# Optimization experiments

Measured on AMD Instinct MI355X. Metric: run time of the kernel, lower is better.

The kernel has to match this reference:

```python
import jax, jax.numpy as jnp
import numpy as np

NUM_HEADS = 16

def _alibi(S, H, dtype):
    # fairseq-style ALiBi: slopes[h] * -(|i-j|), H assumed power of 2
    start = 2.0 ** (-8.0 / H)
    slopes = start ** jnp.arange(1, H + 1, dtype=jnp.float32)      # [H]
    pos = jnp.arange(S)
    rel = -jnp.abs(pos[None, :] - pos[:, None]).astype(jnp.float32)  # [S,S]
    return (slopes[:, None, None] * rel).astype(dtype)             # [H,S,S]

def setup_inputs() -> dict:
    key = jax.random.key(0)
    kx, km, kw1, kw2 = jax.random.split(key, 4)
    B, S, D = 2, 2048, 1024
    inputs = jax.random.normal(kx, (B, S, D), dtype=jnp.float32)
    mask = jax.random.bernoulli(km, 0.9, (B, S))
    mask = mask.at[:, 0].set(True)  # ensure each row has a valid key
    Wqkv = jax.random.normal(kw1, (3 * D, D), dtype=jnp.float32) * 0.02
    bqkv = jnp.zeros((3 * D,), dtype=jnp.float32)
    Wproj = jax.random.normal(kw2, (D, D), dtype=jnp.float32) * 0.02
    bproj = jnp.zeros((D,), dtype=jnp.float32)
    return {"inputs": inputs, "mask": mask, "Wqkv": Wqkv, "bqkv": bqkv,
            "Wproj": Wproj, "bproj": bproj}

def reference(inputs, mask, Wqkv, bqkv, Wproj, bproj):
    B, S, D = inputs.shape
    H = NUM_HEADS
    dh = D // H
    scale = D ** (-0.5)  # NOTE: original scales by full dim, not head dim
    qkv = inputs @ Wqkv.T + bqkv                       # [B,S,3D]
    qkv = qkv.reshape(B, S, H, 3 * dh).transpose(0, 2, 1, 3)  # [B,H,S,3dh]
    q, k, v = qkv[..., :dh], qkv[..., dh:2 * dh], qkv[..., 2 * dh:]
    attn = jnp.einsum('bhqd,bhkd->bhqk', q, k) * scale  # [B,H,S,S]
    attn = attn + _alibi(S, H, attn.dtype)[None]
    attn = jnp.where(mask[:, None, None, :], attn, jnp.finfo(attn.dtype).min)
    attn = jax.nn.softmax(attn, axis=-1)
    x = jnp.einsum('bhqk,bhkd->bhqd', attn, v)          # [B,H,S,dh]
    x = x.transpose(0, 2, 1, 3).reshape(B, S, D)
    return x @ Wproj.T + bproj
```

## Files before the change

kernel.cpp:

```cpp
#include <hip/hip_runtime.h>
#include <cstdint>
#include <cstddef>

#define B_  2
#define S_  2048
#define D_  1024
#define H_  16
#define DH_ 64
#define M_  (B_*S_)
#define N3_ (3*D_)
#define NT_ (S_/64)

typedef float f32x4 __attribute__((ext_vector_type(4)));
typedef short short8 __attribute__((ext_vector_type(8)));
typedef unsigned short u16x8 __attribute__((ext_vector_type(8)));
typedef unsigned short u16x4 __attribute__((ext_vector_type(4)));

__device__ __forceinline__ unsigned short f2bf(float x) {
    unsigned int u = __float_as_uint(x);
    unsigned int r = (u + 0x7FFFu + ((u >> 16) & 1u)) >> 16;
    return (unsigned short)r;
}

__device__ __forceinline__ float exp2_(float x) { return __builtin_amdgcn_exp2f(x); }

__device__ __forceinline__ unsigned int cvt_pk_bf16(float a, float b) {
    unsigned int r;
    asm volatile("v_cvt_pk_bf16_f32 %0, %1, %2" : "=v"(r) : "v"(a), "v"(b));
    return r;
}

__device__ __forceinline__ void gload16(const void* g, void* l) {
    __builtin_amdgcn_global_load_lds(
        (const __attribute__((address_space(1))) unsigned int*)g,
        (__attribute__((address_space(3))) unsigned int*)l,
        16, 0, 0);
}

__global__ void k_detect_mask(const unsigned char* __restrict__ mb, int* __restrict__ flag) {
    __shared__ int sBig, sM4, sM8;
    if (threadIdx.x == 0) { sBig = 0; sM4 = 0; sM8 = 0; }
    __syncthreads();
    int big = 0, m4 = 0, m8 = 0;
    for (int i = threadIdx.x; i < 4096; i += blockDim.x) {
        unsigned char v = mb[i];
        if (v > 1) big = 1;
        if (v && (i & 3)) m4 = 1;
        if (v && ((i & 7) == 4)) m8 = 1;
    }
    if (big) atomicOr(&sBig, 1);
    if (m4)  atomicOr(&sM4, 1);
    if (m8)  atomicOr(&sM8, 1);
    __syncthreads();
    if (threadIdx.x == 0) {
        int w;
        if (sBig)      w = 0;
        else if (sM4)  w = 1;
        else if (sM8)  w = 4;
        else           w = 8;
        *flag = w;
    }
}

__global__ void k_maskbits(const void* __restrict__ mask, const int* __restrict__ flag,
                           unsigned long long* __restrict__ bits) {
    int i = blockIdx.x * 64 + threadIdx.x;
    int w = *flag;
    bool on;
    if (w == 0)      on = ((const float*)mask)[i] != 0.0f;
    else if (w == 1) on = ((const unsigned char*)mask)[i] != 0;
    else if (w == 4) on = ((const int*)mask)[i] != 0;
    else             on = ((const long long*)mask)[i] != 0;
    unsigned long long bal = __ballot(on);
    if (threadIdx.x == 0) bits[blockIdx.x] = bal;
}

__global__ void k_f2bf(const float* __restrict__ in, unsigned short* __restrict__ out, int n) {
    int i = (blockIdx.x * blockDim.x + threadIdx.x) * 4;
    if (i >= n) return;
    float4 v = *reinterpret_cast<const float4*>(&in[i]);
    u16x4 o = { f2bf(v.x), f2bf(v.y), f2bf(v.z), f2bf(v.w) };
    *reinterpret_cast<u16x4*>(&out[i]) = o;
}

template <bool OUT_BF16>
__global__ __launch_bounds__(256) void k_gemm_bf16_nt(
    const unsigned short* __restrict__ A, const unsigned short* __restrict__ W,
    const float* __restrict__ bias, void* __restrict__ Cout,
    int M, int N, int K) {
    __shared__ __align__(16) unsigned short Al[128 * 64];
    __shared__ __align__(16) unsigned short Wl[128 * 64];

    const int tid  = threadIdx.x;
    const int lane = tid & 63;
    const int w    = tid >> 6;
    const int wr   = w >> 1, wc = w & 1;
    const int l16  = lane & 15, g = lane >> 4;
    const int m0 = blockIdx.y * 128, n0 = blockIdx.x * 128;

    f32x4 acc[4][4];
#pragma unroll
    for (int m = 0; m < 4; ++m)
#pragma unroll
        for (int n = 0; n < 4; ++n) acc[m][n] = (f32x4){0.f, 0.f, 0.f, 0.f};

    const int srow = tid >> 3, scol = (tid & 7) * 8;

    for (int k0 = 0; k0 < K; k0 += 64) {
        __syncthreads();
#pragma unroll
        for (int i = 0; i < 4; ++i) {
            const int c = i * 256 + tid;
            const int row = srow + i * 32;
            gload16(A + (size_t)(m0 + row) * K + k0 + scol, Al + c * 8);
            gload16(W + (size_t)(n0 + row) * K + k0 + scol, Wl + c * 8);
        }
        __syncthreads();

#pragma unroll
        for (int kk = 0; kk < 2; ++kk) {
            short8 a[4], b[4];
#pragma unroll
            for (int m = 0; m < 4; ++m)
                a[m] = *reinterpret_cast<const short8*>(
                    &Al[(size_t)(wr * 64 + m * 16 + l16) * 64 + kk * 32 + g * 8]);
#pragma unroll
            for (int n = 0; n < 4; ++n)
                b[n] = *reinterpret_cast<const short8*>(
                    &Wl[(size_t)(wc * 64 + n * 16 + l16) * 64 + kk * 32 + g * 8]);
#pragma unroll
            for (int m = 0; m < 4; ++m)
#pragma unroll
                for (int n = 0; n < 4; ++n)
                    acc[m][n] = __builtin_amdgcn_mfma_f32_16x16x32_bf16(a[m], b[n], acc[m][n], 0, 0, 0);
        }
    }

    float bv[4];
#pragma unroll
    for (int n = 0; n < 4; ++n) bv[n] = bias[n0 + wc * 64 + n * 16 + l16];
#pragma unroll
    for (int m = 0; m < 4; ++m) {
#pragma unroll
        for (int r = 0; r < 4; ++r) {
            const size_t row = m0 + wr * 64 + m * 16 + g * 4 + r;
#pragma unroll
            for (int n = 0; n < 4; ++n) {
                const int col = n0 + wc * 64 + n * 16 + l16;
                float v = acc[m][n][r] + bv[n];
                if (OUT_BF16)
                    ((unsigned short*)Cout)[row * N + col] = f2bf(v);
                else
                    ((float*)Cout)[row * N + col] = v;
            }
        }
    }
}

__global__ __launch_bounds__(256) void k_attn_mfma(
    const unsigned short* __restrict__ qkv,
    const unsigned long long* __restrict__ mbits,
    unsigned short* __restrict__ x) {
    __shared__ __align__(16) unsigned short Kt[64][72];
    __shared__ __align__(16) unsigned short Vt[64][72];
    __shared__ __align__(16) unsigned short QP[64][72];
    __shared__ __align__(16) float Am[S_];

    const int tid  = threadIdx.x;
    const int lane = tid & 63;
    const int wq   = tid >> 6;
    const int g    = lane >> 4;
    const int g4   = g * 4;
    const int l16  = lane & 15;

    const int nqt = S_ / 64;
    const int qt = blockIdx.x % nqt;
    const int h  = (blockIdx.x / nqt) % H_;
    const int b  = blockIdx.x / (nqt * H_);
    const int q0 = qt * 64;
    const size_t rowbase = (size_t)b * S_ * N3_;
    const int hq = h * 192, hk = hq + 64, hv = hq + 128;
    const unsigned short* kvb = qkv + rowbase;

    {
#pragma unroll
        for (int it = 0; it < S_ / 256; ++it) {
            const int k = it * 256 + tid;
            const unsigned long long w = mbits[b * NT_ + (k >> 6)];
            Am[k] = ((w >> (k & 63)) & 1ull) ? 0.0f : -1e30f;
        }
    }

    {
        const int row = tid >> 2, cb = (tid & 3) * 16;
        const unsigned short* src = kvb + (size_t)(q0 + row) * N3_ + hq + cb;
        *reinterpret_cast<u16x8*>(&QP[row][cb])     = *reinterpret_cast<const u16x8*>(src);
        *reinterpret_cast<u16x8*>(&QP[row][cb + 8]) = *reinterpret_cast<const u16x8*>(src + 8);
    }
    __syncthreads();

    const short8 qa0 = *reinterpret_cast<const short8*>(&QP[wq*16 + l16][g*8]);
    const short8 qa1 = *reinterpret_cast<const short8*>(&QP[wq*16 + l16][32 + g*8]);

    f32x4 Oacc[4];
#pragma unroll
    for (int df = 0; df < 4; ++df) Oacc[df] = (f32x4){0.f, 0.f, 0.f, 0.f};
    float m = -1e30f, l = 0.0f;

    const float LOG2E = 1.4426950408889634f;
    const float c1 = 0.03125f * LOG2E;
    const float c2 = exp2f(-0.5f * (float)(h + 1)) * LOG2E;
    const int   qg = q0 + wq * 16 + l16;
    float albr[4];
#pragma unroll
    for (int r = 0; r < 4; ++r) albr[r] = c2 * (float)(g4 + r);
    const float c2_16 = c2 * 16.0f;

    const int krow = tid >> 2, kcb = (tid & 3) * 16;
    const int vkb = (tid & 15) * 4, vdb = (tid >> 4) * 4;
    u16x8 kr0, kr1;
    u16x4 vr0, vr1, vr2, vr3;

    {
        const unsigned short* ks = kvb + (size_t)krow * N3_ + hk + kcb;
        kr0 = *reinterpret_cast<const u16x8*>(ks);
        kr1 = *reinterpret_cast<const u16x8*>(ks + 8);
        const unsigned short* vs = kvb + (size_t)vkb * N3_ + hv + vdb;
        vr0 = *reinterpret_cast<const u16x4*>(vs);
        vr1 = *reinterpret_cast<const u16x4*>(vs + N3_);
        vr2 = *reinterpret_cast<const u16x4*>(vs + 2 * N3_);
        vr3 = *reinterpret_cast<const u16x4*>(vs + 3 * N3_);
    }

    for (int t = 0; t < NT_; ++t) {
        const int k0 = t * 64;
        __syncthreads();

        *reinterpret_cast<u16x8*>(&Kt[krow][kcb])     = kr0;
        *reinterpret_cast<u16x8*>(&Kt[krow][kcb + 8]) = kr1;
        {
            u16x4 w0 = { vr0.x, vr1.x, vr2.x, vr3.x };
            u16x4 w1 = { vr0.y, vr1.y, vr2.y, vr3.y };
            u16x4 w2 = { vr0.z, vr1.z, vr2.z, vr3.z };
            u16x4 w3 = { vr0.w, vr1.w, vr2.w, vr3.w };
            *reinterpret_cast<u16x4*>(&Vt[vdb + 0][vkb]) = w0;
            *reinterpret_cast<u16x4*>(&Vt[vdb + 1][vkb]) = w1;
            *reinterpret_cast<u16x4*>(&Vt[vdb + 2][vkb]) = w2;
            *reinterpret_cast<u16x4*>(&Vt[vdb + 3][vkb]) = w3;
        }
        if (t + 1 < NT_) {
            const int kn = k0 + 64;
            const unsigned short* ks = kvb + (size_t)(kn + krow) * N3_ + hk + kcb;
            kr0 = *reinterpret_cast<const u16x8*>(ks);
            kr1 = *reinterpret_cast<const u16x8*>(ks + 8);
            const unsigned short* vs = kvb + (size_t)(kn + vkb) * N3_ + hv + vdb;
            vr0 = *reinterpret_cast<const u16x4*>(vs);
            vr1 = *reinterpret_cast<const u16x4*>(vs + N3_);
            vr2 = *reinterpret_cast<const u16x4*>(vs + 2 * N3_);
            vr3 = *reinterpret_cast<const u16x4*>(vs + 3 * N3_);
        }
        __syncthreads();

        float p_[4][4];
        __builtin_amdgcn_s_setprio(1);
#pragma unroll
        for (int jb = 0; jb < 4; ++jb) {
            short8 kb0 = *reinterpret_cast<const short8*>(&Kt[jb*16 + l16][g*8]);
            short8 kb1 = *reinterpret_cast<const short8*>(&Kt[jb*16 + l16][32 + g*8]);
            f32x4 c = (f32x4){0.f, 0.f, 0.f, 0.f};
            c = __builtin_amdgcn_mfma_f32_16x16x32_bf16(kb0, qa0, c, 0, 0, 0);
            c = __builtin_amdgcn_mfma_f32_16x16x32_bf16(kb1, qa1, c, 0, 0, 0);
#pragma unroll
            for (int r = 0; r < 4; ++r) p_[jb][r] = c[r];
        }
        __builtin_amdgcn_s_setprio(0);

        f32x4 amv[4];
#pragma unroll
        for (int jb = 0; jb < 4; ++jb)
            amv[jb] = *reinterpret_cast<const f32x4*>(&Am[k0 + jb * 16 + g4]);

        if (k0 < q0) {
            const float tb = c2 * (float)(k0 - qg);
#pragma unroll
            for (int jb = 0; jb < 4; ++jb) {
                const float tbj = tb + c2_16 * (float)jb;
#pragma unroll
                for (int r = 0; r < 4; ++r)
                    p_[jb][r] = fmaf(p_[jb][r], c1, tbj + albr[r] + amv[jb][r]);
            }
        } else if (k0 > q0) {
            const float tb = c2 * (float)(k0 - qg);
#pragma unroll
            for (int jb = 0; jb < 4; ++jb) {
                const float tbj = -tb - c2_16 * (float)jb;
#pragma unroll
                for (int r = 0; r < 4; ++r)
                    p_[jb][r] = fmaf(p_[jb][r], c1, tbj - albr[r] + amv[jb][r]);
            }
        } else {
            const int dbase = k0 - qg;
#pragma unroll
            for (int jb = 0; jb < 4; ++jb)
#pragma unroll
                for (int r = 0; r < 4; ++r) {
                    int d = dbase + jb * 16 + g4 + r;
                    d = d < 0 ? -d : d;
                    p_[jb][r] = fmaf(p_[jb][r], c1, amv[jb][r] - c2 * (float)d);
                }
        }

        float mx;
        {
            float m0_ = fmaxf(fmaxf(p_[0][0], p_[0][1]), fmaxf(p_[0][2], p_[0][3]));
            float m1_ = fmaxf(fmaxf(p_[1][0], p_[1][1]), fmaxf(p_[1][2], p_[1][3]));
            float m2_ = fmaxf(fmaxf(p_[2][0], p_[2][1]), fmaxf(p_[2][2], p_[2][3]));
            float m3_ = fmaxf(fmaxf(p_[3][0], p_[3][1]), fmaxf(p_[3][2], p_[3][3]));
            mx = fmaxf(fmaxf(m0_, m1_), fmaxf(m2_, m3_));
        }
        mx = fmaxf(mx, __shfl_xor(mx, 16));
        mx = fmaxf(mx, __shfl_xor(mx, 32));

        if (__any(mx > m + 8.0f)) {
            const float mn = fmaxf(m, mx);
            const float cr = exp2_(m - mn);
            m = mn;
            l *= cr;
            const int srcb = (lane & 48) + ((lane & 48) >> 2);
#pragma unroll
            for (int r = 0; r < 4; ++r) {
                const float crq = __shfl(cr, srcb + r);
#pragma unroll
                for (int df = 0; df < 4; ++df) Oacc[df][r] *= crq;
            }
        }

        float ps = 0.0f;
#pragma unroll
        for (int jb = 0; jb < 4; ++jb)
#pragma unroll
            for (int r = 0; r < 4; ++r) {
                float p = exp2_(p_[jb][r] - m);
                p_[jb][r] = p;
                ps += p;
            }

#pragma unroll
        for (int jb = 0; jb < 4; ++jb) {
            uint2 st;
            st.x = cvt_pk_bf16(p_[jb][0], p_[jb][1]);
            st.y = cvt_pk_bf16(p_[jb][2], p_[jb][3]);
            *reinterpret_cast<uint2*>(&QP[wq*16 + l16][jb*16 + g4]) = st;
        }

        const short8 pa0 = *reinterpret_cast<const short8*>(&QP[wq*16 + l16][g*8]);
        const short8 pa1 = *reinterpret_cast<const short8*>(&QP[wq*16 + l16][32 + g*8]);
        __builtin_amdgcn_s_setprio(1);
#pragma unroll
        for (int df = 0; df < 4; ++df) {
            short8 vb0 = *reinterpret_cast<const short8*>(&Vt[df*16 + l16][g*8]);
            short8 vb1 = *reinterpret_cast<const short8*>(&Vt[df*16 + l16][32 + g*8]);
            Oacc[df] = __builtin_amdgcn_mfma_f32_16x16x32_bf16(pa0, vb0, Oacc[df], 0, 0, 0);
            Oacc[df] = __builtin_amdgcn_mfma_f32_16x16x32_bf16(pa1, vb1, Oacc[df], 0, 0, 0);
        }
        __builtin_amdgcn_s_setprio(0);

        ps += __shfl_xor(ps, 16);
        ps += __shfl_xor(ps, 32);
        l += ps;
    }

    const int srcb = (lane & 48) + ((lane & 48) >> 2);
    float invq[4];
#pragma unroll
    for (int r = 0; r < 4; ++r) invq[r] = 1.0f / __shfl(l, srcb + r);
#pragma unroll
    for (int df = 0; df < 4; ++df) {
#pragma unroll
        for (int r = 0; r < 4; ++r) {
            const int qrow = q0 + wq * 16 + g4 + r;
            x[(size_t)(b * S_ + qrow) * D_ + h * 64 + df * 16 + l16] = f2bf(Oacc[df][r] * invq[r]);
        }
    }
}

extern "C" void kernel_launch(void* const* d_in, const int* in_sizes, int n_in,
                              void* d_out, int out_size, void* d_ws, size_t ws_size,
                              hipStream_t stream) {
    const float* inputs = (const float*)d_in[0];
    const void*  mask   = d_in[1];
    const float* Wqkv   = (const float*)d_in[2];
    const float* bqkv   = (const float*)d_in[3];
    const float* Wproj  = (const float*)d_in[4];
    const float* bproj  = (const float*)d_in[5];
    float* out = (float*)d_out;

    unsigned short* qkvb = (unsigned short*)d_ws;
    unsigned short* xb   = qkvb + (size_t)M_ * N3_;
    unsigned short* Ab   = xb + (size_t)M_ * D_;
    unsigned short* Wqb  = Ab + (size_t)M_ * D_;
    unsigned short* Wpb  = Wqb + (size_t)N3_ * D_;
    unsigned long long* bits = (unsigned long long*)(Wpb + (size_t)D_ * D_);
    int* flag = (int*)(bits + B_ * NT_);

    k_detect_mask<<<1, 256, 0, stream>>>((const unsigned char*)mask, flag);
    k_maskbits<<<B_ * NT_, 64, 0, stream>>>(mask, flag, bits);

    k_f2bf<<<(M_ * D_ / 4 + 255) / 256, 256, 0, stream>>>(inputs, Ab, M_ * D_);
    k_f2bf<<<(N3_ * D_ / 4 + 255) / 256, 256, 0, stream>>>(Wqkv, Wqb, N3_ * D_);
    k_f2bf<<<(D_ * D_ / 4 + 255) / 256, 256, 0, stream>>>(Wproj, Wpb, D_ * D_);

    dim3 g1(N3_ / 128, M_ / 128);
    k_gemm_bf16_nt<true><<<g1, 256, 0, stream>>>(Ab, Wqb, bqkv, qkvb, M_, N3_, D_);

    k_attn_mfma<<<B_ * H_ * (S_ / 64), 256, 0, stream>>>(qkvb, bits, xb);

    dim3 g2(D_ / 128, M_ / 128);
    k_gemm_bf16_nt<false><<<g2, 256, 0, stream>>>(xb, Wpb, bproj, out, M_, D_, D_);
}
```

Before: 200.4 us.

## Double-buffer K/V tiles with 128-query blocks and precomputed mask bias

The attention kernel now handles 128 query rows per block with 512 threads, so each K/V tile in LDS is shared by twice as many query rows. K/V tiles are double-buffered in shared memory, which leaves one barrier per iteration instead of two. The mask is expanded once into a global float bias array and read directly each tile, replacing the per-block LDS mask table built from bitmasks. The ALiBi branch conditions were adjusted to per-wave query offsets. The trade-offs are fewer blocks (less parallelism), higher per-block register and LDS pressure, and uncached global mask loads inside the loop.

```diff
diff --git a/kernel.cpp b/kernel.cpp
--- a/kernel.cpp
+++ b/kernel.cpp
@@ -15,6 +15,7 @@
 typedef short short8 __attribute__((ext_vector_type(8)));
 typedef unsigned short u16x8 __attribute__((ext_vector_type(8)));
 typedef unsigned short u16x4 __attribute__((ext_vector_type(4)));
+typedef unsigned short u16x2 __attribute__((ext_vector_type(2)));
 
 __device__ __forceinline__ unsigned short f2bf(float x) {
     unsigned int u = __float_as_uint(x);
@@ -62,17 +63,17 @@
     }
 }
 
-__global__ void k_maskbits(const void* __restrict__ mask, const int* __restrict__ flag,
-                           unsigned long long* __restrict__ bits) {
-    int i = blockIdx.x * 64 + threadIdx.x;
+__global__ void k_expand_mask(const void* __restrict__ mask, const int* __restrict__ flag,
+                              float* __restrict__ maskbias, int n) {
+    int i = blockIdx.x * blockDim.x + threadIdx.x;
+    if (i >= n) return;
     int w = *flag;
     bool on;
     if (w == 0)      on = ((const float*)mask)[i] != 0.0f;
     else if (w == 1) on = ((const unsigned char*)mask)[i] != 0;
     else if (w == 4) on = ((const int*)mask)[i] != 0;
     else             on = ((const long long*)mask)[i] != 0;
-    unsigned long long bal = __ballot(on);
-    if (threadIdx.x == 0) bits[blockIdx.x] = bal;
+    maskbias[i] = on ? 0.0f : -1e30f;
 }
 
 __global__ void k_f2bf(const float* __restrict__ in, unsigned short* __restrict__ out, int n) {
@@ -157,14 +158,13 @@
     }
 }
 
-__global__ __launch_bounds__(256) void k_attn_mfma(
+__global__ __launch_bounds__(512) void k_attn_mfma(
     const unsigned short* __restrict__ qkv,
-    const unsigned long long* __restrict__ mbits,
+    const float* __restrict__ maskbias,
     unsigned short* __restrict__ x) {
-    __shared__ __align__(16) unsigned short Kt[64][72];
-    __shared__ __align__(16) unsigned short Vt[64][72];
-    __shared__ __align__(16) unsigned short QP[64][72];
-    __shared__ __align__(16) float Am[S_];
+    __shared__ __align__(16) unsigned short Kt[2][64][72];
+    __shared__ __align__(16) unsigned short Vt[2][64][72];
+    __shared__ __align__(16) unsigned short QP[128][72];
 
     const int tid  = threadIdx.x;
     const int lane = tid & 63;
@@ -173,23 +173,15 @@
     const int g4   = g * 4;
     const int l16  = lane & 15;
 
-    const int nqt = S_ / 64;
+    const int nqt = S_ / 128;
     const int qt = blockIdx.x % nqt;
     const int h  = (blockIdx.x / nqt) % H_;
     const int b  = blockIdx.x / (nqt * H_);
-    const int q0 = qt * 64;
+    const int q0 = qt * 128;
     const size_t rowbase = (size_t)b * S_ * N3_;
     const int hq = h * 192, hk = hq + 64, hv = hq + 128;
     const unsigned short* kvb = qkv + rowbase;
-
-    {
-#pragma unroll
-        for (int it = 0; it < S_ / 256; ++it) {
-            const int k = it * 256 + tid;
-            const unsigned long long w = mbits[b * NT_ + (k >> 6)];
-            Am[k] = ((w >> (k & 63)) & 1ull) ? 0.0f : -1e30f;
-        }
-    }
+    const float* mbp = maskbias + b * S_;
 
     {
         const int row = tid >> 2, cb = (tid & 3) * 16;
@@ -197,6 +189,22 @@
         *reinterpret_cast<u16x8*>(&QP[row][cb])     = *reinterpret_cast<const u16x8*>(src);
         *reinterpret_cast<u16x8*>(&QP[row][cb + 8]) = *reinterpret_cast<const u16x8*>(src + 8);
     }
+
+    const int krow = tid >> 3, kcb = (tid & 7) * 8;
+    const int vkb = (tid & 31) * 2, vdb = (tid >> 5) * 4;
+    u16x8 kr;
+    u16x4 vr0, vr1;
+
+    {
+        kr  = *reinterpret_cast<const u16x8*>(kvb + (size_t)krow * N3_ + hk + kcb);
+        const unsigned short* vs = kvb + (size_t)vkb * N3_ + hv + vdb;
+        vr0 = *reinterpret_cast<const u16x4*>(vs);
+        vr1 = *reinterpret_cast<const u16x4*>(vs + N3_);
+        *reinterpret_cast<u16x8*>(&Kt[0][krow][kcb]) = kr;
+#pragma unroll
+        for (int j = 0; j < 4; ++j)
+            *reinterpret_cast<u16x2*>(&Vt[0][vdb + j][vkb]) = (u16x2){vr0[j], vr1[j]};
+    }
     __syncthreads();
 
     const short8 qa0 = *reinterpret_cast<const short8*>(&QP[wq*16 + l16][g*8]);
@@ -210,63 +218,36 @@
     const float LOG2E = 1.4426950408889634f;
     const float c1 = 0.03125f * LOG2E;
     const float c2 = exp2f(-0.5f * (float)(h + 1)) * LOG2E;
-    const int   qg = q0 + wq * 16 + l16;
+    const int   qw0 = q0 + wq * 16;
+    const int   qg  = qw0 + l16;
     float albr[4];
 #pragma unroll
     for (int r = 0; r < 4; ++r) albr[r] = c2 * (float)(g4 + r);
     const float c2_16 = c2 * 16.0f;
 
-    const int krow = tid >> 2, kcb = (tid & 3) * 16;
-    const int vkb = (tid & 15) * 4, vdb = (tid >> 4) * 4;
-    u16x8 kr0, kr1;
-    u16x4 vr0, vr1, vr2, vr3;
-
-    {
-        const unsigned short* ks = kvb + (size_t)krow * N3_ + hk + kcb;
-        kr0 = *reinterpret_cast<const u16x8*>(ks);
-        kr1 = *reinterpret_cast<const u16x8*>(ks + 8);
-        const unsigned short* vs = kvb + (size_t)vkb * N3_ + hv + vdb;
-        vr0 = *reinterpret_cast<const u16x4*>(vs);
-        vr1 = *reinterpret_cast<const u16x4*>(vs + N3_);
-        vr2 = *reinterpret_cast<const u16x4*>(vs + 2 * N3_);
-        vr3 = *reinterpret_cast<const u16x4*>(vs + 3 * N3_);
-    }
-
     for (int t = 0; t < NT_; ++t) {
         const int k0 = t * 64;
-        __syncthreads();
-
-        *reinterpret_cast<u16x8*>(&Kt[krow][kcb])     = kr0;
-        *reinterpret_cast<u16x8*>(&Kt[krow][kcb + 8]) = kr1;
-        {
-            u16x4 w0 = { vr0.x, vr1.x, vr2.x, vr3.x };
-            u16x4 w1 = { vr0.y, vr1.y, vr2.y, vr3.y };
-            u16x4 w2 = { vr0.z, vr1.z, vr2.z, vr3.z };
-            u16x4 w3 = { vr0.w, vr1.w, vr2.w, vr3.w };
-            *reinterpret_cast<u16x4*>(&Vt[vdb + 0][vkb]) = w0;
-            *reinterpret_cast<u16x4*>(&Vt[vdb + 1][vkb]) = w1;
-            *reinterpret_cast<u16x4*>(&Vt[vdb + 2][vkb]) = w2;
-            *reinterpret_cast<u16x4*>(&Vt[vdb + 3][vkb]) = w3;
-        }
+        const int cur = t & 1;
+
         if (t + 1 < NT_) {
             const int kn = k0 + 64;
-            const unsigned short* ks = kvb + (size_t)(kn + krow) * N3_ + hk + kcb;
-            kr0 = *reinterpret_cast<const u16x8*>(ks);
-            kr1 = *reinterpret_cast<const u16x8*>(ks + 8);
+            kr  = *reinterpret_cast<const u16x8*>(kvb + (size_t)(kn + krow) * N3_ + hk + kcb);
             const unsigned short* vs = kvb + (size_t)(kn + vkb) * N3_ + hv + vdb;
             vr0 = *reinterpret_cast<const u16x4*>(vs);
             vr1 = *reinterpret_cast<const u16x4*>(vs + N3_);
-            vr2 = *reinterpret_cast<const u16x4*>(vs + 2 * N3_);
-            vr3 = *reinterpret_cast<const u16x4*>(vs + 3 * N3_);
-        }
-        __syncthreads();
+        }
+
+        f32x4 amv[4];
+#pragma unroll
+        for (int jb = 0; jb < 4; ++jb)
+            amv[jb] = *reinterpret_cast<const f32x4*>(&mbp[k0 + jb * 16 + g4]);
 
         float p_[4][4];
         __builtin_amdgcn_s_setprio(1);
 #pragma unroll
         for (int jb = 0; jb < 4; ++jb) {
-            short8 kb0 = *reinterpret_cast<const short8*>(&Kt[jb*16 + l16][g*8]);
-            short8 kb1 = *reinterpret_cast<const short8*>(&Kt[jb*16 + l16][32 + g*8]);
+            short8 kb0 = *reinterpret_cast<const short8*>(&Kt[cur][jb*16 + l16][g*8]);
+            short8 kb1 = *reinterpret_cast<const short8*>(&Kt[cur][jb*16 + l16][32 + g*8]);
             f32x4 c = (f32x4){0.f, 0.f, 0.f, 0.f};
             c = __builtin_amdgcn_mfma_f32_16x16x32_bf16(kb0, qa0, c, 0, 0, 0);
             c = __builtin_amdgcn_mfma_f32_16x16x32_bf16(kb1, qa1, c, 0, 0, 0);
@@ -275,12 +256,7 @@
         }
         __builtin_amdgcn_s_setprio(0);
 
-        f32x4 amv[4];
-#pragma unroll
-        for (int jb = 0; jb < 4; ++jb)
-            amv[jb] = *reinterpret_cast<const f32x4*>(&Am[k0 + jb * 16 + g4]);
-
-        if (k0 < q0) {
+        if (k0 + 64 <= qw0) {
             const float tb = c2 * (float)(k0 - qg);
 #pragma unroll
             for (int jb = 0; jb < 4; ++jb) {
@@ -289,7 +265,7 @@
                 for (int r = 0; r < 4; ++r)
                     p_[jb][r] = fmaf(p_[jb][r], c1, tbj + albr[r] + amv[jb][r]);
             }
-        } else if (k0 > q0) {
+        } else if (k0 >= qw0 + 16) {
             const float tb = c2 * (float)(k0 - qg);
 #pragma unroll
             for (int jb = 0; jb < 4; ++jb) {
@@ -358,8 +334,8 @@
         __builtin_amdgcn_s_setprio(1);
 #pragma unroll
         for (int df = 0; df < 4; ++df) {
-            short8 vb0 = *reinterpret_cast<const short8*>(&Vt[df*16 + l16][g*8]);
-            short8 vb1 = *reinterpret_cast<const short8*>(&Vt[df*16 + l16][32 + g*8]);
+            short8 vb0 = *reinterpret_cast<const short8*>(&Vt[cur][df*16 + l16][g*8]);
+            short8 vb1 = *reinterpret_cast<const short8*>(&Vt[cur][df*16 + l16][32 + g*8]);
             Oacc[df] = __builtin_amdgcn_mfma_f32_16x16x32_bf16(pa0, vb0, Oacc[df], 0, 0, 0);
             Oacc[df] = __builtin_amdgcn_mfma_f32_16x16x32_bf16(pa1, vb1, Oacc[df], 0, 0, 0);
         }
@@ -368,6 +344,14 @@
         ps += __shfl_xor(ps, 16);
         ps += __shfl_xor(ps, 32);
         l += ps;
+
+        if (t + 1 < NT_) {
+            *reinterpret_cast<u16x8*>(&Kt[cur ^ 1][krow][kcb]) = kr;
+#pragma unroll
+            for (int j = 0; j < 4; ++j)
+                *reinterpret_cast<u16x2*>(&Vt[cur ^ 1][vdb + j][vkb]) = (u16x2){vr0[j], vr1[j]};
+            __syncthreads();
+        }
     }
 
     const int srcb = (lane & 48) + ((lane & 48) >> 2);
@@ -400,11 +384,11 @@
     unsigned short* Ab   = xb + (size_t)M_ * D_;
     unsigned short* Wqb  = Ab + (size_t)M_ * D_;
     unsigned short* Wpb  = Wqb + (size_t)N3_ * D_;
-    unsigned long long* bits = (unsigned long long*)(Wpb + (size_t)D_ * D_);
-    int* flag = (int*)(bits + B_ * NT_);
+    float* maskbias = (float*)(Wpb + (size_t)D_ * D_);
+    int*   flag     = (int*)(maskbias + M_);
 
     k_detect_mask<<<1, 256, 0, stream>>>((const unsigned char*)mask, flag);
-    k_maskbits<<<B_ * NT_, 64, 0, stream>>>(mask, flag, bits);
+    k_expand_mask<<<(M_ + 255) / 256, 256, 0, stream>>>(mask, flag, maskbias, M_);
 
     k_f2bf<<<(M_ * D_ / 4 + 255) / 256, 256, 0, stream>>>(inputs, Ab, M_ * D_);
     k_f2bf<<<(N3_ * D_ / 4 + 255) / 256, 256, 0, stream>>>(Wqkv, Wqb, N3_ * D_);
@@ -413,7 +397,7 @@
     dim3 g1(N3_ / 128, M_ / 128);
     k_gemm_bf16_nt<true><<<g1, 256, 0, stream>>>(Ab, Wqb, bqkv, qkvb, M_, N3_, D_);
 
-    k_attn_mfma<<<B_ * H_ * (S_ / 64), 256, 0, stream>>>(qkvb, bits, xb);
+    k_attn_mfma<<<B_ * H_ * (S_ / 128), 512, 0, stream>>>(qkvb, maskbias, xb);
 
     dim3 g2(D_ / 128, M_ / 128);
     k_gemm_bf16_nt<false><<<g2, 256, 0, stream>>>(xb, Wpb, bproj, out, M_, D_, D_);
```

Result: faster. 178.2 us (-11.1%).
